# Optimization experiments

Measured on AMD Instinct MI355X. Metric: run time of the kernel, lower is better.

## Reference

```python
import jax, jax.numpy as jnp
import numpy as np

BATCH = 8192
IN_F = 1024
OUT_F = 1024
GRID_SIZE = 5
SPLINE_ORDER = 3
GRID_LO, GRID_HI = -1.0, 1.0


def setup_inputs() -> dict:
    key = jax.random.key(0)
    k1, k2, k3, k4 = jax.random.split(key, 4)
    x = jax.random.normal(k1, (BATCH, IN_F), dtype=jnp.float32)
    # grid buffer: extended knot vector, same for every input feature
    h = (GRID_HI - GRID_LO) / GRID_SIZE
    knots = jnp.linspace(GRID_LO - SPLINE_ORDER * h, GRID_HI + SPLINE_ORDER * h,
                         GRID_SIZE + 2 * SPLINE_ORDER + 1, dtype=jnp.float32)
    grid = jnp.tile(knots[None, :], (IN_F, 1))  # [in, 12]
    fan_in_scale = 1.0 / np.sqrt(IN_F)
    base_weight = jax.random.normal(k2, (OUT_F, IN_F), dtype=jnp.float32) * fan_in_scale
    spline_weight = jax.random.normal(k3, (IN_F, GRID_SIZE + SPLINE_ORDER, OUT_F), dtype=jnp.float32) * 0.1
    spline_scaler = jax.random.normal(k4, (IN_F, OUT_F), dtype=jnp.float32) * fan_in_scale
    return {"x": x, "grid": grid, "base_weight": base_weight,
            "spline_weight": spline_weight, "spline_scaler": spline_scaler}


def b_splines(x, grid):
    """Cox-de Boor recursion. x: [B, in], grid: [in, G+2k+1] -> [B, in, G+k]."""
    xe = x[:, :, None]  # [B, in, 1]
    bases = ((xe >= grid[:, :-1]) & (xe < grid[:, 1:])).astype(x.dtype)  # [B, in, G+2k]
    for k in range(1, SPLINE_ORDER + 1):
        left = (xe - grid[:, :-(k + 1)]) / (grid[:, k:-1] - grid[:, :-(k + 1)])
        right = (grid[:, k + 1:] - xe) / (grid[:, k + 1:] - grid[:, 1:-k])
        bases = left * bases[:, :, :-1] + right * bases[:, :, 1:]
    return bases  # [B, in, G+k]


def reference(x, grid, base_weight, spline_weight, spline_scaler):
    # base branch: SiLU(x) @ W_base^T
    base_out = jax.nn.silu(x) @ base_weight.T  # [B, out]
    # spline branch
    basis = b_splines(x, grid)  # [B, in, G+k]
    scaled_w = spline_weight * spline_scaler[:, None, :]  # [in, G+k, out]
    spline_out = jnp.einsum('bik,iko->bo', basis, scaled_w)  # [B, out]
    return base_out + spline_out
```

## Files before the change

kernel.cpp:

```cpp
#include <hip/hip_runtime.h>
#include <cstdint>
#include <cstddef>

#define BATCH 8192
#define IN_F 1024
#define OUT_F 1024
#define NSPL 9
#define KDIM (IN_F * NSPL)

typedef __bf16 bf16x8 __attribute__((ext_vector_type(8)));
typedef __bf16 bf16x4 __attribute__((ext_vector_type(4)));
typedef float f32x4 __attribute__((ext_vector_type(4)));

__device__ __forceinline__ void g2l16(const void* g, void* l) {
  __builtin_amdgcn_global_load_lds(
      (__attribute__((address_space(1))) void*)(g),
      (__attribute__((address_space(3))) void*)(l),
      16, 0, 0);
}

__global__ __launch_bounds__(256) void build_w(const float* __restrict__ bw,
                                               const float* __restrict__ sw,
                                               const float* __restrict__ sc,
                                               __bf16* __restrict__ Wt) {
  __shared__ float s_sw[16 * 8 * 64];
  __shared__ float s_sc[16 * 64];
  __shared__ float s_bw[64 * 16];
  const int tid = threadIdx.x;
  const int o0 = (blockIdx.x & 15) * 64;
  const int i0 = (blockIdx.x >> 4) * 16;

#pragma unroll
  for (int it = 0; it < 32; ++it) {
    const int t = it * 256 + tid;
    const int i = t >> 9, r = (t >> 6) & 7, oo = t & 63;
    s_sw[t] = sw[((size_t)(i0 + i) * 8 + r) * OUT_F + o0 + oo];
  }
#pragma unroll
  for (int it = 0; it < 4; ++it) {
    const int t = it * 256 + tid;
    const int i = t >> 6, oo = t & 63;
    s_sc[t] = sc[(size_t)(i0 + i) * OUT_F + o0 + oo];
  }
#pragma unroll
  for (int it = 0; it < 4; ++it) {
    const int t = it * 256 + tid;
    const int oo = t >> 4, ii = t & 15;
    s_bw[t] = bw[(size_t)(o0 + oo) * IN_F + i0 + ii];
  }
  __syncthreads();

  const int oo = tid >> 2;
  const int ig = (tid & 3) * 4;
  __bf16* orow = Wt + (size_t)(o0 + oo) * KDIM;

  {
    bf16x4 v;
#pragma unroll
    for (int e = 0; e < 4; ++e) v[e] = (__bf16)s_bw[oo * 16 + ig + e];
    *(bf16x4*)(orow + i0 + ig) = v;
  }
#pragma unroll
  for (int r = 0; r < 8; ++r) {
    bf16x4 v;
#pragma unroll
    for (int e = 0; e < 4; ++e) {
      const int i = ig + e;
      v[e] = (__bf16)(s_sw[i * 512 + r * 64 + oo] * s_sc[i * 64 + oo]);
    }
    *(bf16x4*)(orow + (r + 1) * 1024 + i0 + ig) = v;
  }
}

__global__ __launch_bounds__(256) void build_a(const float* __restrict__ x,
                                               __bf16* __restrict__ A) {
  const int b = blockIdx.x;
  const int tid = threadIdx.x;
  const int i0 = tid * 4;
  const float4 v4 = ((const float4*)(x + (size_t)b * IN_F))[tid];
  const float vs[4] = {v4.x, v4.y, v4.z, v4.w};
  __bf16* dst = A + (size_t)b * KDIM;

  {
    bf16x4 s;
#pragma unroll
    for (int e = 0; e < 4; ++e) {
      const float v = vs[e];
      s[e] = (__bf16)(v / (1.f + __expf(-v)));
    }
    *(bf16x4*)(dst + i0) = s;
  }

  float c0[4], c1[4], c2[4], c3[4];
  int cel[4];
#pragma unroll
  for (int e = 0; e < 4; ++e) {
    const float p = (vs[e] + 2.2f) * 2.5f;
    const float fc = floorf(p);
    cel[e] = (int)fc;
    const float t = p - fc;
    const float t2 = t * t, t3 = t2 * t, omt = 1.f - t;
    c0[e] = (1.f / 6.f) * omt * omt * omt;
    c1[e] = (1.f / 6.f) * (3.f * t3 - 6.f * t2 + 4.f);
    c2[e] = (1.f / 6.f) * (-3.f * t3 + 3.f * t2 + 3.f * t + 1.f);
    c3[e] = (1.f / 6.f) * t3;
  }

#pragma unroll
  for (int j = 0; j < 8; ++j) {
    bf16x4 v;
#pragma unroll
    for (int e = 0; e < 4; ++e) {
      const int d = j - cel[e] + 3;
      const float w = (d == 0) ? c0[e]
                    : (d == 1) ? c1[e]
                    : (d == 2) ? c2[e]
                    : (d == 3) ? c3[e]
                               : 0.f;
      v[e] = (__bf16)w;
    }
    *(bf16x4*)(dst + (j + 1) * 1024 + i0) = v;
  }
}

__global__ __launch_bounds__(256) void gemm_bt(const __bf16* __restrict__ A,
                                               const __bf16* __restrict__ W,
                                               float* __restrict__ out) {
  __shared__ __align__(16) __bf16 As[2 * 128 * 32];
  __shared__ __align__(16) __bf16 Bs[2 * 128 * 32];

  const int tid = threadIdx.x;
  const int wv = tid >> 6;
  const int lane = tid & 63;
  const int mb = blockIdx.x & 63;
  const int nb = blockIdx.x >> 6;
  const int m0 = mb * 128;
  const int n0 = nb * 128;
  const int wr = wv & 1;
  const int wc = wv >> 1;

  const int srow = lane >> 2;
  const int scol = (lane & 3) * 8;
  const __bf16* gA = A + (size_t)(m0 + wv * 32 + srow) * KDIM + scol;
  const __bf16* gB = W + (size_t)(n0 + wv * 32 + srow) * KDIM + scol;
  __bf16* lA = As + wv * 1024;
  __bf16* lB = Bs + wv * 1024;

  const int mrow = lane & 15;
  const int quad = lane >> 4;
  int aoff[4], boff[4];
#pragma unroll
  for (int mt = 0; mt < 4; ++mt) aoff[mt] = (wr * 64 + mt * 16 + mrow) * 32 + quad * 8;
#pragma unroll
  for (int nt = 0; nt < 4; ++nt) boff[nt] = (wc * 64 + nt * 16 + mrow) * 32 + quad * 8;

  f32x4 acc[4][4];
  const f32x4 zero = {0.f, 0.f, 0.f, 0.f};
#pragma unroll
  for (int mt = 0; mt < 4; ++mt)
#pragma unroll
    for (int nt = 0; nt < 4; ++nt) acc[mt][nt] = zero;

  for (int k0 = 0; k0 < KDIM; k0 += 64) {
    __syncthreads();
    g2l16(gA + k0, lA);
    g2l16(gA + k0 + (size_t)16 * KDIM, lA + 512);
    g2l16(gB + k0, lB);
    g2l16(gB + k0 + (size_t)16 * KDIM, lB + 512);
    g2l16(gA + k0 + 32, lA + 4096);
    g2l16(gA + k0 + 32 + (size_t)16 * KDIM, lA + 4096 + 512);
    g2l16(gB + k0 + 32, lB + 4096);
    g2l16(gB + k0 + 32 + (size_t)16 * KDIM, lB + 4096 + 512);
    __syncthreads();

    bf16x8 af[2][4], bfr[2][4];
#pragma unroll
    for (int h = 0; h < 2; ++h) {
#pragma unroll
      for (int mt = 0; mt < 4; ++mt) af[h][mt] = *(const bf16x8*)(As + h * 4096 + aoff[mt]);
#pragma unroll
      for (int nt = 0; nt < 4; ++nt) bfr[h][nt] = *(const bf16x8*)(Bs + h * 4096 + boff[nt]);
    }
#pragma unroll
    for (int h = 0; h < 2; ++h)
#pragma unroll
      for (int mt = 0; mt < 4; ++mt)
#pragma unroll
        for (int nt = 0; nt < 4; ++nt)
          acc[mt][nt] = __builtin_amdgcn_mfma_f32_16x16x32_bf16(af[h][mt], bfr[h][nt],
                                                                acc[mt][nt], 0, 0, 0);
  }

#pragma unroll
  for (int mt = 0; mt < 4; ++mt) {
#pragma unroll
    for (int nt = 0; nt < 4; ++nt) {
      const int col = n0 + wc * 64 + nt * 16 + mrow;
      const int rbase = m0 + wr * 64 + mt * 16 + quad * 4;
#pragma unroll
      for (int r = 0; r < 4; ++r)
        out[(size_t)(rbase + r) * OUT_F + col] = acc[mt][nt][r];
    }
  }
}

extern "C" void kernel_launch(void* const* d_in, const int* in_sizes, int n_in,
                              void* d_out, int out_size, void* d_ws, size_t ws_size,
                              hipStream_t stream) {
  const float* x  = (const float*)d_in[0];
  const float* bw = (const float*)d_in[2];
  const float* sw = (const float*)d_in[3];
  const float* sc = (const float*)d_in[4];
  float* out = (float*)d_out;

  __bf16* Wt = (__bf16*)d_ws;
  __bf16* Ab = (__bf16*)((char*)d_ws +
                         (size_t)OUT_F * KDIM * sizeof(__bf16));

  build_w<<<1024, 256, 0, stream>>>(bw, sw, sc, Wt);
  build_a<<<BATCH, 256, 0, stream>>>(x, Ab);
  gemm_bt<<<(BATCH / 128) * (OUT_F / 128), 256, 0, stream>>>(Ab, Wt, out);
}
```

Baseline: 317.4 us.

## Fuse weight build, activation build and GEMM into one persistent kernel

Merges the three kernels (build_w, build_a, gemm_bt) into a single 512-block kernel. Each block first builds 16 rows of the activation matrix and two tiles of the bf16 weight matrix, then waits at a grid-wide atomic-counter barrier before running its GEMM tile. This removes two kernel launch boundaries and their tail gaps, at the cost of a memset launch and a spin barrier. The barrier relies on all 512 blocks being co-resident (launch_bounds 256,2), or it can deadlock. The prep phases also run with fewer blocks than before, which may lower their parallelism.

```diff
diff --git a/kernel.cpp b/kernel.cpp
--- a/kernel.cpp
+++ b/kernel.cpp
@@ -7,6 +7,7 @@
 #define OUT_F 1024
 #define NSPL 9
 #define KDIM (IN_F * NSPL)
+#define NBLK 512
 
 typedef __bf16 bf16x8 __attribute__((ext_vector_type(8)));
 typedef __bf16 bf16x4 __attribute__((ext_vector_type(4)));
@@ -19,121 +20,130 @@
       16, 0, 0);
 }
 
-__global__ __launch_bounds__(256) void build_w(const float* __restrict__ bw,
-                                               const float* __restrict__ sw,
-                                               const float* __restrict__ sc,
-                                               __bf16* __restrict__ Wt) {
-  __shared__ float s_sw[16 * 8 * 64];
-  __shared__ float s_sc[16 * 64];
-  __shared__ float s_bw[64 * 16];
+__global__ __launch_bounds__(256, 2) void kan_fused(
+    const float* __restrict__ x, const float* __restrict__ bw,
+    const float* __restrict__ sw, const float* __restrict__ sc,
+    __bf16* __restrict__ Wt, __bf16* __restrict__ Ab,
+    float* __restrict__ out, unsigned* __restrict__ ctr) {
+  __shared__ __align__(16) char smem[40960];
   const int tid = threadIdx.x;
-  const int o0 = (blockIdx.x & 15) * 64;
-  const int i0 = (blockIdx.x >> 4) * 16;
-
-#pragma unroll
-  for (int it = 0; it < 32; ++it) {
-    const int t = it * 256 + tid;
-    const int i = t >> 9, r = (t >> 6) & 7, oo = t & 63;
-    s_sw[t] = sw[((size_t)(i0 + i) * 8 + r) * OUT_F + o0 + oo];
-  }
-#pragma unroll
-  for (int it = 0; it < 4; ++it) {
-    const int t = it * 256 + tid;
-    const int i = t >> 6, oo = t & 63;
-    s_sc[t] = sc[(size_t)(i0 + i) * OUT_F + o0 + oo];
-  }
-#pragma unroll
-  for (int it = 0; it < 4; ++it) {
-    const int t = it * 256 + tid;
-    const int oo = t >> 4, ii = t & 15;
-    s_bw[t] = bw[(size_t)(o0 + oo) * IN_F + i0 + ii];
-  }
+  const int bid = blockIdx.x;
+
+  {
+    const int i0 = tid * 4;
+    for (int rr = 0; rr < 16; ++rr) {
+      const int b = bid * 16 + rr;
+      const float4 v4 = ((const float4*)(x + (size_t)b * IN_F))[tid];
+      const float vs[4] = {v4.x, v4.y, v4.z, v4.w};
+      __bf16* dst = Ab + (size_t)b * KDIM;
+
+      {
+        bf16x4 s;
+#pragma unroll
+        for (int e = 0; e < 4; ++e) {
+          const float v = vs[e];
+          s[e] = (__bf16)(v / (1.f + __expf(-v)));
+        }
+        *(bf16x4*)(dst + i0) = s;
+      }
+      float c0[4], c1[4], c2[4], c3[4];
+      int cel[4];
+#pragma unroll
+      for (int e = 0; e < 4; ++e) {
+        const float p = (vs[e] + 2.2f) * 2.5f;
+        const float fc = floorf(p);
+        cel[e] = (int)fc;
+        const float t = p - fc;
+        const float t2 = t * t, t3 = t2 * t, omt = 1.f - t;
+        c0[e] = (1.f / 6.f) * omt * omt * omt;
+        c1[e] = (1.f / 6.f) * (3.f * t3 - 6.f * t2 + 4.f);
+        c2[e] = (1.f / 6.f) * (-3.f * t3 + 3.f * t2 + 3.f * t + 1.f);
+        c3[e] = (1.f / 6.f) * t3;
+      }
+#pragma unroll
+      for (int j = 0; j < 8; ++j) {
+        bf16x4 v;
+#pragma unroll
+        for (int e = 0; e < 4; ++e) {
+          const int d = j - cel[e] + 3;
+          const float w = (d == 0) ? c0[e]
+                        : (d == 1) ? c1[e]
+                        : (d == 2) ? c2[e]
+                        : (d == 3) ? c3[e]
+                                   : 0.f;
+          v[e] = (__bf16)w;
+        }
+        *(bf16x4*)(dst + (j + 1) * 1024 + i0) = v;
+      }
+    }
+  }
+
+  {
+    float* s_sw = (float*)smem;
+    float* s_sc = (float*)(smem + 32768);
+    float* s_bw = (float*)(smem + 36864);
+    for (int ob = 0; ob < 2; ++ob) {
+      const int obid = bid * 2 + ob;
+      const int o0 = (obid & 15) * 64;
+      const int i0 = (obid >> 4) * 16;
+      __syncthreads();
+#pragma unroll
+      for (int it = 0; it < 32; ++it) {
+        const int t = it * 256 + tid;
+        const int i = t >> 9, r = (t >> 6) & 7, oo = t & 63;
+        s_sw[t] = sw[((size_t)(i0 + i) * 8 + r) * OUT_F + o0 + oo];
+      }
+#pragma unroll
+      for (int it = 0; it < 4; ++it) {
+        const int t = it * 256 + tid;
+        const int i = t >> 6, oo = t & 63;
+        s_sc[t] = sc[(size_t)(i0 + i) * OUT_F + o0 + oo];
+      }
+#pragma unroll
+      for (int it = 0; it < 4; ++it) {
+        const int t = it * 256 + tid;
+        const int oo = t >> 4, ii = t & 15;
+        s_bw[t] = bw[(size_t)(o0 + oo) * IN_F + i0 + ii];
+      }
+      __syncthreads();
+      const int oo = tid >> 2;
+      const int ig = (tid & 3) * 4;
+      __bf16* orow = Wt + (size_t)(o0 + oo) * KDIM;
+      {
+        bf16x4 v;
+#pragma unroll
+        for (int e = 0; e < 4; ++e) v[e] = (__bf16)s_bw[oo * 16 + ig + e];
+        *(bf16x4*)(orow + i0 + ig) = v;
+      }
+#pragma unroll
+      for (int r = 0; r < 8; ++r) {
+        bf16x4 v;
+#pragma unroll
+        for (int e = 0; e < 4; ++e) {
+          const int i = ig + e;
+          v[e] = (__bf16)(s_sw[i * 512 + r * 64 + oo] * s_sc[i * 64 + oo]);
+        }
+        *(bf16x4*)(orow + (r + 1) * 1024 + i0 + ig) = v;
+      }
+    }
+  }
+
   __syncthreads();
-
-  const int oo = tid >> 2;
-  const int ig = (tid & 3) * 4;
-  __bf16* orow = Wt + (size_t)(o0 + oo) * KDIM;
-
-  {
-    bf16x4 v;
-#pragma unroll
-    for (int e = 0; e < 4; ++e) v[e] = (__bf16)s_bw[oo * 16 + ig + e];
-    *(bf16x4*)(orow + i0 + ig) = v;
-  }
-#pragma unroll
-  for (int r = 0; r < 8; ++r) {
-    bf16x4 v;
-#pragma unroll
-    for (int e = 0; e < 4; ++e) {
-      const int i = ig + e;
-      v[e] = (__bf16)(s_sw[i * 512 + r * 64 + oo] * s_sc[i * 64 + oo]);
-    }
-    *(bf16x4*)(orow + (r + 1) * 1024 + i0 + ig) = v;
-  }
-}
-
-__global__ __launch_bounds__(256) void build_a(const float* __restrict__ x,
-                                               __bf16* __restrict__ A) {
-  const int b = blockIdx.x;
-  const int tid = threadIdx.x;
-  const int i0 = tid * 4;
-  const float4 v4 = ((const float4*)(x + (size_t)b * IN_F))[tid];
-  const float vs[4] = {v4.x, v4.y, v4.z, v4.w};
-  __bf16* dst = A + (size_t)b * KDIM;
-
-  {
-    bf16x4 s;
-#pragma unroll
-    for (int e = 0; e < 4; ++e) {
-      const float v = vs[e];
-      s[e] = (__bf16)(v / (1.f + __expf(-v)));
-    }
-    *(bf16x4*)(dst + i0) = s;
-  }
-
-  float c0[4], c1[4], c2[4], c3[4];
-  int cel[4];
-#pragma unroll
-  for (int e = 0; e < 4; ++e) {
-    const float p = (vs[e] + 2.2f) * 2.5f;
-    const float fc = floorf(p);
-    cel[e] = (int)fc;
-    const float t = p - fc;
-    const float t2 = t * t, t3 = t2 * t, omt = 1.f - t;
-    c0[e] = (1.f / 6.f) * omt * omt * omt;
-    c1[e] = (1.f / 6.f) * (3.f * t3 - 6.f * t2 + 4.f);
-    c2[e] = (1.f / 6.f) * (-3.f * t3 + 3.f * t2 + 3.f * t + 1.f);
-    c3[e] = (1.f / 6.f) * t3;
-  }
-
-#pragma unroll
-  for (int j = 0; j < 8; ++j) {
-    bf16x4 v;
-#pragma unroll
-    for (int e = 0; e < 4; ++e) {
-      const int d = j - cel[e] + 3;
-      const float w = (d == 0) ? c0[e]
-                    : (d == 1) ? c1[e]
-                    : (d == 2) ? c2[e]
-                    : (d == 3) ? c3[e]
-                               : 0.f;
-      v[e] = (__bf16)w;
-    }
-    *(bf16x4*)(dst + (j + 1) * 1024 + i0) = v;
-  }
-}
-
-__global__ __launch_bounds__(256) void gemm_bt(const __bf16* __restrict__ A,
-                                               const __bf16* __restrict__ W,
-                                               float* __restrict__ out) {
-  __shared__ __align__(16) __bf16 As[2 * 128 * 32];
-  __shared__ __align__(16) __bf16 Bs[2 * 128 * 32];
-
-  const int tid = threadIdx.x;
+  if (tid == 0) {
+    __hip_atomic_fetch_add(ctr, 1u, __ATOMIC_ACQ_REL, __HIP_MEMORY_SCOPE_AGENT);
+    while (__hip_atomic_load(ctr, __ATOMIC_ACQUIRE, __HIP_MEMORY_SCOPE_AGENT) <
+           (unsigned)NBLK)
+      __builtin_amdgcn_s_sleep(4);
+  }
+  __syncthreads();
+
+  __bf16* As = (__bf16*)smem;
+  __bf16* Bs = (__bf16*)(smem + 16384);
+
   const int wv = tid >> 6;
   const int lane = tid & 63;
-  const int mb = blockIdx.x & 63;
-  const int nb = blockIdx.x >> 6;
+  const int mb = bid & 63;
+  const int nb = bid >> 6;
   const int m0 = mb * 128;
   const int n0 = nb * 128;
   const int wr = wv & 1;
@@ -141,8 +151,8 @@
 
   const int srow = lane >> 2;
   const int scol = (lane & 3) * 8;
-  const __bf16* gA = A + (size_t)(m0 + wv * 32 + srow) * KDIM + scol;
-  const __bf16* gB = W + (size_t)(n0 + wv * 32 + srow) * KDIM + scol;
+  const __bf16* gA = Ab + (size_t)(m0 + wv * 32 + srow) * KDIM + scol;
+  const __bf16* gB = Wt + (size_t)(n0 + wv * 32 + srow) * KDIM + scol;
   __bf16* lA = As + wv * 1024;
   __bf16* lB = Bs + wv * 1024;
 
@@ -216,8 +226,9 @@
   __bf16* Wt = (__bf16*)d_ws;
   __bf16* Ab = (__bf16*)((char*)d_ws +
                          (size_t)OUT_F * KDIM * sizeof(__bf16));
-
-  build_w<<<1024, 256, 0, stream>>>(bw, sw, sc, Wt);
-  build_a<<<BATCH, 256, 0, stream>>>(x, Ab);
-  gemm_bt<<<(BATCH / 128) * (OUT_F / 128), 256, 0, stream>>>(Ab, Wt, out);
+  unsigned* ctr = (unsigned*)((char*)d_ws +
+                              (size_t)(OUT_F + BATCH) * KDIM * sizeof(__bf16));
+
+  hipMemsetAsync(ctr, 0, 64, stream);
+  kan_fused<<<NBLK, 256, 0, stream>>>(x, bw, sw, sc, Wt, Ab, out, ctr);
 }
```

New measurement: 438.7 us. 1.38x slower.
